# Kernel tuning notes

Measured on AMD Instinct MI355X. Metric: run time of the kernel, lower is better.

Reference implementation:

```python
import jax, jax.numpy as jnp
import numpy as np

TAU = 1.0
BASE = 7
NUM_TWISTS = 3
EPS = 1e-6

B, S, D, P, M = 4, 2048, 1024, 9, 256


def _rot(y, theta):
    # learned rotation in the (0,1) channel plane; theta broadcasts against y[..., 0]
    c, s = jnp.cos(theta), jnp.sin(theta)
    y0, y1 = y[..., 0], y[..., 1]
    r0 = (y0 * c - y1 * s)[..., None]
    r1 = (y0 * s + y1 * c)[..., None]
    return jnp.concatenate([r0, r1, y[..., 2:]], axis=-1)


def _mod_phase_norm(x, g, base=BASE):
    # RMS-normalize within channel groups defined by (channel index mod base)
    d = x.shape[-1]
    gid = jnp.arange(d) % base
    oh = jax.nn.one_hot(gid, base, dtype=x.dtype)           # [d, base]
    cnt = oh.sum(axis=0)                                    # [base]
    msq = (x * x) @ oh / cnt                                # [..., base]
    denom = jnp.sqrt(jnp.take(msq, gid, axis=-1) + EPS)     # [..., d]
    return x / denom * g


def setup_inputs() -> dict:
    key = jax.random.key(0)
    ks = jax.random.split(key, 16)
    w = lambda k, shape, scale: jax.random.normal(k, shape, dtype=jnp.float32) * scale
    u = jax.random.uniform(ks[1], (NUM_TWISTS + 1, B, S, P), dtype=jnp.float32,
                           minval=1e-6, maxval=1.0 - 1e-6)
    gumbel_noise = -jnp.log(-jnp.log(u))
    return {
        'x': w(ks[0], (B, S, D), 1.0),
        'gumbel_noise': gumbel_noise,
        'mixer_w': w(ks[2], (3, D), 0.5),
        'obs_W1': w(ks[3], (2 * D, M), (2 * D) ** -0.5),
        'obs_b1': jnp.zeros((M,), jnp.float32),
        'obs_th1': w(ks[4], (), 0.1),
        'obs_W2': w(ks[5], (M, P), M ** -0.5),
        'obs_b2': jnp.zeros((P,), jnp.float32),
        'obs_th2': w(ks[6], (), 0.1),
        'path_Wa': w(ks[7], (P, D, M), D ** -0.5),
        'path_ba': jnp.zeros((P, M), jnp.float32),
        'path_tha': w(ks[8], (P,), 0.1),
        'path_Wb': w(ks[9], (P, M, D), M ** -0.5),
        'path_bb': jnp.zeros((P, D), jnp.float32),
        'path_thb': w(ks[10], (P,), 0.1),
        'twist_W': w(ks[11], (D, D), D ** -0.5),
        'twist_b': jnp.zeros((D,), jnp.float32),
        'twist_th': w(ks[12], (), 0.1),
        'norm_g': jnp.ones((D,), jnp.float32),
    }


def reference(x, gumbel_noise, mixer_w, obs_W1, obs_b1, obs_th1, obs_W2, obs_b2,
              obs_th2, path_Wa, path_ba, path_tha, path_Wb, path_bb, path_thb,
              twist_W, twist_b, twist_th, norm_g):
    # neighbor mixer: per-channel 3-tap mix over sequence (zero-padded, non-causal)
    xp = jnp.pad(x, ((0, 0), (1, 1), (0, 0)))
    x_mixed = x * mixer_w[0] + xp[:, :-2] * mixer_w[1] + xp[:, 2:] * mixer_w[2]

    def observer_logits(collapsed):
        combined = jnp.concatenate([x_mixed, collapsed], axis=-1)      # [B,S,2D]
        h = jnp.tanh(_rot(combined @ obs_W1 + obs_b1, obs_th1))        # [B,S,M]
        return _rot(h @ obs_W2 + obs_b2, obs_th2)                      # [B,S,P]

    def path_outputs_fn(tin):
        h = _rot(jnp.einsum('bsd,pdm->bspm', tin, path_Wa) + path_ba, path_tha)
        return _rot(jnp.einsum('bspm,pmd->bspd', h, path_Wb) + path_bb, path_thb)

    collapsed = jnp.zeros_like(x_mixed)
    path_out = None
    for t in range(NUM_TWISTS):
        logits = observer_logits(collapsed)
        rw = jax.nn.softmax((logits + gumbel_noise[t]) / TAU, axis=-1)  # soft gumbel
        tin = x_mixed + _rot(collapsed @ twist_W + twist_b, twist_th)
        path_out = path_outputs_fn(tin)                                # [B,S,P,D]
        collapsed = _mod_phase_norm(jnp.einsum('bspd,bsp->bsd', path_out, rw), norm_g)

    # final hard (straight-through) gumbel routing, reusing last path_out
    final_logits = observer_logits(collapsed)
    soft = jax.nn.softmax((final_logits + gumbel_noise[NUM_TWISTS]) / TAU, axis=-1)
    hard = jax.nn.one_hot(jnp.argmax(soft, axis=-1), P, dtype=soft.dtype)
    rw_hard = hard + soft - jax.lax.stop_gradient(soft)
    final_collapsed = jnp.einsum('bspd,bsp->bsd', path_out, rw_hard)

    # dropout is identity in eval mode
    out = _mod_phase_norm(x + final_collapsed, norm_g)
    collapsed = _mod_phase_norm(collapsed, norm_g)
    return out, collapsed
```

## Files before the change

### kernel.cpp

```cpp
#include <hip/hip_runtime.h>
#include <hip/hip_bf16.h>

typedef unsigned short u16;
typedef short bf16x8 __attribute__((ext_vector_type(8)));
typedef float f32x4 __attribute__((ext_vector_type(4)));

constexpr int Dd = 1024, Pp = 9, Mm = 256, Nn = 8192, Kc = 2304;
constexpr float EPSf = 1e-6f;

__device__ __forceinline__ float bf2f(u16 u) {
    union { unsigned int u; float f; } v; v.u = ((unsigned int)u) << 16; return v.f;
}
__device__ __forceinline__ u16 f2bf(float f) {
    union { float f; unsigned int u; } v; v.f = f;
    unsigned int r = (v.u + 0x7FFFu + ((v.u >> 16) & 1u)) >> 16; return (u16)r;
}
__device__ __forceinline__ void split2(float v, u16& h, u16& l) {
    h = f2bf(v); l = f2bf(v - bf2f(h));
}
__device__ __forceinline__ void gld16(u16* lds, const u16* g) {
    __builtin_amdgcn_global_load_lds(
        (const __attribute__((address_space(1))) unsigned int*)g,
        (__attribute__((address_space(3))) unsigned int*)lds, 16, 0, 0);
}

__global__ void rotcopy_k(const float* __restrict__ src, float* __restrict__ dst,
                          int R, int C, const float* __restrict__ theta, int Pb)
{
    long total = (long)Pb * R * C;
    long idx = (long)blockIdx.x * 256 + threadIdx.x;
    if (idx >= total) return;
    int c = (int)(idx % C);
    long rp = idx / C;
    int r = (int)(rp % R);
    int pb = (int)(rp / R);
    float th = theta[pb];
    const float* s = src + ((long)pb * R + r) * C;
    float v;
    if (c == 0)      v = s[0] * cosf(th) - s[1] * sinf(th);
    else if (c == 1) v = s[0] * sinf(th) + s[1] * cosf(th);
    else             v = s[c];
    dst[idx] = v;
}

__global__ void splitW1_k(const float* __restrict__ W1, const float* __restrict__ th,
                          u16* __restrict__ h, u16* __restrict__ l)
{
    int idx = blockIdx.x * 256 + threadIdx.x;
    if (idx >= 256 * 2048) return;
    int k = idx & 2047, n = idx >> 11;
    float v;
    if (n == 0)      v = W1[(long)k * 256 + 0] * cosf(th[0]) - W1[(long)k * 256 + 1] * sinf(th[0]);
    else if (n == 1) v = W1[(long)k * 256 + 0] * sinf(th[0]) + W1[(long)k * 256 + 1] * cosf(th[0]);
    else             v = W1[(long)k * 256 + n];
    u16 hh, ll; split2(v, hh, ll); h[idx] = hh; l[idx] = ll;
}

__global__ void splitTW_k(const float* __restrict__ tW, const float* __restrict__ th,
                          u16* __restrict__ h, u16* __restrict__ l)
{
    int idx = blockIdx.x * 256 + threadIdx.x;
    if (idx >= 1024 * 1024) return;
    int k = idx & 1023, n = idx >> 10;
    float v;
    if (n == 0)      v = tW[(long)k * 1024 + 0] * cosf(th[0]) - tW[(long)k * 1024 + 1] * sinf(th[0]);
    else if (n == 1) v = tW[(long)k * 1024 + 0] * sinf(th[0]) + tW[(long)k * 1024 + 1] * cosf(th[0]);
    else             v = tW[(long)k * 1024 + n];
    u16 hh, ll; split2(v, hh, ll); h[idx] = hh; l[idx] = ll;
}

__global__ void splitWa_k(const float* __restrict__ Wa, const float* __restrict__ tha,
                          u16* __restrict__ h, u16* __restrict__ l)
{
    int idx = blockIdx.x * 256 + threadIdx.x;
    if (idx >= Kc * 1024) return;
    int k = idx & 1023, n = idx >> 10;
    int p = n >> 8, m = n & 255;
    const float* s = Wa + ((long)p * 1024 + k) * 256;
    float v;
    if (m == 0)      v = s[0] * cosf(tha[p]) - s[1] * sinf(tha[p]);
    else if (m == 1) v = s[0] * sinf(tha[p]) + s[1] * cosf(tha[p]);
    else             v = s[m];
    u16 hh, ll; split2(v, hh, ll); h[idx] = hh; l[idx] = ll;
}

__global__ void splitWb_k(const float* __restrict__ Wb, const float* __restrict__ thb,
                          u16* __restrict__ h, u16* __restrict__ l)
{
    int idx = blockIdx.x * 256 + threadIdx.x;
    if (idx >= 1024 * Kc) return;
    int n = idx / Kc;
    int k = idx - n * Kc;
    int p = k >> 8, m = k & 255;
    const float* s = Wb + ((long)p * 256 + m) * 1024;
    float v;
    if (n == 0)      v = s[0] * cosf(thb[p]) - s[1] * sinf(thb[p]);
    else if (n == 1) v = s[0] * sinf(thb[p]) + s[1] * cosf(thb[p]);
    else             v = s[n];
    u16 hh, ll; split2(v, hh, ll); h[idx] = hh; l[idx] = ll;
}

__global__ void mixer_k(const float* __restrict__ x, const float* __restrict__ mw,
                        u16* __restrict__ xmh, u16* __restrict__ xml)
{
    int idx = blockIdx.x * 256 + threadIdx.x;
    if (idx >= Nn * Dd / 4) return;
    int d4 = idx & (Dd / 4 - 1);
    int n = idx >> 8;
    int s = n & 2047;
    const float4* x4 = (const float4*)x;
    const float4* w4 = (const float4*)mw;
    float4 xc = x4[idx];
    float4 w0 = w4[d4], w1 = w4[(Dd / 4) + d4], w2 = w4[2 * (Dd / 4) + d4];
    float o[4];
    o[0] = xc.x * w0.x; o[1] = xc.y * w0.y; o[2] = xc.z * w0.z; o[3] = xc.w * w0.w;
    if (s > 0) {
        float4 xl = x4[idx - Dd / 4];
        o[0] += xl.x * w1.x; o[1] += xl.y * w1.y; o[2] += xl.z * w1.z; o[3] += xl.w * w1.w;
    }
    if (s < 2047) {
        float4 xr = x4[idx + Dd / 4];
        o[0] += xr.x * w2.x; o[1] += xr.y * w2.y; o[2] += xr.z * w2.z; o[3] += xr.w * w2.w;
    }
    ushort4 h4, l4;
    split2(o[0], h4.x, l4.x); split2(o[1], h4.y, l4.y);
    split2(o[2], h4.z, l4.z); split2(o[3], h4.w, l4.w);
    ((ushort4*)xmh)[idx] = h4; ((ushort4*)xml)[idx] = l4;
}

__global__ void tanh_k(const float* __restrict__ a, float* __restrict__ o, int total)
{
    int idx = blockIdx.x * 256 + threadIdx.x;
    if (idx < total) o[idx] = tanhf(a[idx]);
}

__global__ void addb_split_k(const u16* __restrict__ xmh, const u16* __restrict__ xml,
                             const float* __restrict__ tbr,
                             u16* __restrict__ th_, u16* __restrict__ tl_)
{
    int idx = blockIdx.x * 256 + threadIdx.x;
    if (idx >= Nn * Dd / 4) return;
    int d4 = idx & (Dd / 4 - 1);
    ushort4 xh = ((const ushort4*)xmh)[idx], xl = ((const ushort4*)xml)[idx];
    float4 b = ((const float4*)tbr)[d4];
    ushort4 h4, l4;
    split2(bf2f(xh.x) + bf2f(xl.x) + b.x, h4.x, l4.x);
    split2(bf2f(xh.y) + bf2f(xl.y) + b.y, h4.y, l4.y);
    split2(bf2f(xh.z) + bf2f(xl.z) + b.z, h4.z, l4.z);
    split2(bf2f(xh.w) + bf2f(xl.w) + b.w, h4.w, l4.w);
    ((ushort4*)th_)[idx] = h4; ((ushort4*)tl_)[idx] = l4;
}

template<int EPI>
__global__ __launch_bounds__(256, (EPI == 4) ? 2 : 3) void mgemm(
    const u16* __restrict__ Agh, const u16* __restrict__ Agl, int lda,
    const u16* __restrict__ Bgh, const u16* __restrict__ Bgl, int ldb,
    int K,
    float* __restrict__ Cf, u16* __restrict__ Coh, u16* __restrict__ Col, int ldc,
    const float* __restrict__ Cinit,
    const u16* __restrict__ CIh, const u16* __restrict__ CIl,
    const float* __restrict__ bias,
    const float* __restrict__ rwv,
    const float* __restrict__ rwv2,
    const float* __restrict__ bbrv)
{
    __shared__ u16 smem[16384];
    u16* As_h = smem;        u16* As_l = smem + 4096;
    u16* Bs_h = smem + 8192; u16* Bs_l = smem + 12288;
    const int tid = threadIdx.x, wave = tid >> 6, lane = tid & 63;
    const int nwg = gridDim.x * gridDim.y;
    const int flat = blockIdx.y * gridDim.x + blockIdx.x;
    const int q = nwg >> 3;
    const int l_ = (flat & 7) * q + (flat >> 3);
    const int r0 = (l_ / gridDim.x) * 128, c0 = (l_ % gridDim.x) * 128;
    const int srl = lane >> 2;
    const int ssl = ((lane & 3) ^ ((lane >> 3) & 3)) * 8;
    const int frl = lane & 15, kh = lane >> 4;
    const int sw  = (kh ^ ((frl >> 1) & 3)) * 8;
    const int arow0 = (wave >> 1) * 64, bcol0 = (wave & 1) * 64;
    const int w32 = wave * 32;

    f32x4 acc[4][4] = {};

    auto kstep = [&](f32x4 (&ac)[4][4], int k0) {
        {
            const long ga0 = (long)(r0 + w32 + srl) * lda + k0 + ssl;
            gld16(&As_h[w32 * 32],        Agh + ga0);
            gld16(&As_h[(w32 + 16) * 32], Agh + ga0 + 16L * lda);
            gld16(&As_l[w32 * 32],        Agl + ga0);
            gld16(&As_l[(w32 + 16) * 32], Agl + ga0 + 16L * lda);
            const long gb0 = (long)(c0 + w32 + srl) * ldb + k0 + ssl;
            gld16(&Bs_h[w32 * 32],        Bgh + gb0);
            gld16(&Bs_h[(w32 + 16) * 32], Bgh + gb0 + 16L * ldb);
            gld16(&Bs_l[w32 * 32],        Bgl + gb0);
            gld16(&Bs_l[(w32 + 16) * 32], Bgl + gb0 + 16L * ldb);
        }
        __syncthreads();
        bf16x8 ah[4], al[4];
#pragma unroll
        for (int f = 0; f < 4; ++f) {
            int ao = (arow0 + f * 16 + frl) * 32 + sw;
            ah[f] = *(const bf16x8*)&As_h[ao];
            al[f] = *(const bf16x8*)&As_l[ao];
        }
#pragma unroll
        for (int j = 0; j < 4; ++j) {
            int bo = (bcol0 + j * 16 + frl) * 32 + sw;
            bf16x8 bh = *(const bf16x8*)&Bs_h[bo];
            bf16x8 bl = *(const bf16x8*)&Bs_l[bo];
#pragma unroll
            for (int i = 0; i < 4; ++i) {
                ac[i][j] = __builtin_amdgcn_mfma_f32_16x16x32_bf16(ah[i], bh, ac[i][j], 0, 0, 0);
                ac[i][j] = __builtin_amdgcn_mfma_f32_16x16x32_bf16(ah[i], bl, ac[i][j], 0, 0, 0);
                ac[i][j] = __builtin_amdgcn_mfma_f32_16x16x32_bf16(al[i], bh, ac[i][j], 0, 0, 0);
            }
        }
        __syncthreads();
    };

    if constexpr (EPI == 4) {
#pragma unroll 1
        for (int p = 0; p < 9; ++p) {
            f32x4 acc2[4][4] = {};
#pragma unroll 1
            for (int ks = 0; ks < 8; ++ks) kstep(acc2, p * 256 + ks * 32);
#pragma unroll
            for (int i = 0; i < 4; ++i)
#pragma unroll
                for (int reg = 0; reg < 4; ++reg) {
                    float w = rwv[(long)(r0 + arow0 + i * 16 + kh * 4 + reg) * 9 + p];
#pragma unroll
                    for (int j = 0; j < 4; ++j) acc[i][j][reg] += w * acc2[i][j][reg];
                }
        }
    } else {
#pragma unroll 1
        for (int k0 = 0; k0 < K; k0 += 32) kstep(acc, k0);
    }

#pragma unroll
    for (int i = 0; i < 4; ++i)
#pragma unroll
        for (int reg = 0; reg < 4; ++reg) {
            const int r = r0 + arow0 + i * 16 + kh * 4 + reg;
#pragma unroll
            for (int j = 0; j < 4; ++j) {
                const int c = c0 + bcol0 + j * 16 + frl;
                float v = acc[i][j][reg];
                if constexpr (EPI == 0) {
                    Cf[(long)r * ldc + c] = v + bias[c];
                } else if constexpr (EPI == 1) {
                    Cf[(long)r * ldc + c] = tanhf(v + Cinit[(long)r * ldc + c]);
                } else if constexpr (EPI == 2) {
                    long o = (long)r * ldc + c;
                    v += bf2f(CIh[o]) + bf2f(CIl[o]) + bias[c];
                    u16 h, l; split2(v, h, l); Coh[o] = h; Col[o] = l;
                } else if constexpr (EPI == 3) {
                    long o = (long)r * ldc + c;
                    v = (v + bias[c]) * rwv[(long)r * 9 + (c >> 8)];
                    u16 h, l; split2(v, h, l); Coh[o] = h; Col[o] = l;
                } else if constexpr (EPI == 4) {
#pragma unroll
                    for (int p = 0; p < 9; ++p) v += rwv2[(long)r * 9 + p] * bbrv[p * 1024 + c];
                    Cf[(long)r * ldc + c] = v;
                } else {
#pragma unroll
                    for (int p = 0; p < 9; ++p) v += rwv[(long)r * 9 + p] * bbrv[p * 1024 + c];
                    Cf[(long)r * ldc + c] = v;
                }
            }
        }
}

__global__ void logits_k(const float* __restrict__ h, const float* __restrict__ W2r,
                         const float* __restrict__ b2r, const float* __restrict__ gum,
                         float* __restrict__ rwA, float* __restrict__ rwH,
                         const float* __restrict__ rwS, int hard)
{
    __shared__ float hs[Mm];
    __shared__ float lg[16];
    int n = blockIdx.x;
    for (int i = threadIdx.x; i < Mm; i += 64) hs[i] = h[(long)n * Mm + i];
    __syncthreads();
    if (threadIdx.x < Pp) {
        int p = threadIdx.x;
        float acc = b2r[p];
        for (int m = 0; m < Mm; ++m) acc += hs[m] * W2r[m * Pp + p];
        lg[p] = acc + gum[(long)n * Pp + p];
    }
    __syncthreads();
    if (threadIdx.x == 0) {
        float mx = lg[0]; int am = 0;
#pragma unroll
        for (int p = 1; p < Pp; ++p) if (lg[p] > mx) { mx = lg[p]; am = p; }
        if (hard) {
#pragma unroll
            for (int p = 0; p < Pp; ++p) {
                rwA[(long)n * Pp + p] = (p == am) ? 1.f / rwS[(long)n * Pp + p] : 0.f;
                rwH[(long)n * Pp + p] = (p == am) ? 1.f : 0.f;
            }
        } else {
            float e[Pp]; float ssum = 0.f;
#pragma unroll
            for (int p = 0; p < Pp; ++p) { e[p] = expf(lg[p] - mx); ssum += e[p]; }
#pragma unroll
            for (int p = 0; p < Pp; ++p) rwA[(long)n * Pp + p] = e[p] / ssum;
        }
    }
}

template<int INSPLIT, int OUTSPLIT>
__global__ void norm_k(const float* __restrict__ in,
                       const u16* __restrict__ inh, const u16* __restrict__ inl,
                       const float* __restrict__ add, const float* __restrict__ g,
                       float* __restrict__ outf, u16* __restrict__ oh, u16* __restrict__ ol)
{
    __shared__ float sb[256][8];
    __shared__ float dn[8];
    int n = blockIdx.x;
    int t = threadIdx.x;
    float v[4];
#pragma unroll
    for (int j = 0; j < 7; ++j) sb[t][j] = 0.f;
#pragma unroll
    for (int i = 0; i < 4; ++i) {
        int d = t + i * 256;
        long o = (long)n * Dd + d;
        float xv = INSPLIT ? (bf2f(inh[o]) + bf2f(inl[o])) : in[o];
        if (add) xv += add[o];
        v[i] = xv;
        sb[t][d % 7] += xv * xv;
    }
    __syncthreads();
    for (int st = 128; st >= 1; st >>= 1) {
        if (t < st) {
#pragma unroll
            for (int j = 0; j < 7; ++j) sb[t][j] += sb[t + st][j];
        }
        __syncthreads();
    }
    if (t < 7) {
        const float cnt = (t < 2) ? 147.f : 146.f;
        dn[t] = 1.f / sqrtf(sb[0][t] / cnt + EPSf);
    }
    __syncthreads();
#pragma unroll
    for (int i = 0; i < 4; ++i) {
        int d = t + i * 256;
        long o = (long)n * Dd + d;
        float ov = v[i] * dn[d % 7] * g[d];
        if (OUTSPLIT) { u16 h, l; split2(ov, h, l); oh[o] = h; ol[o] = l; }
        else outf[o] = ov;
    }
}

static inline int cdiv(long a, long b) { return (int)((a + b - 1) / b); }

extern "C" void kernel_launch(void* const* d_in, const int* in_sizes, int n_in,
                              void* d_out, int out_size, void* d_ws, size_t ws_size,
                              hipStream_t stream)
{
    const float* x    = (const float*)d_in[0];
    const float* gum  = (const float*)d_in[1];
    const float* mw   = (const float*)d_in[2];
    const float* W1   = (const float*)d_in[3];
    const float* b1   = (const float*)d_in[4];
    const float* th1  = (const float*)d_in[5];
    const float* W2   = (const float*)d_in[6];
    const float* b2   = (const float*)d_in[7];
    const float* th2  = (const float*)d_in[8];
    const float* Wa   = (const float*)d_in[9];
    const float* ba   = (const float*)d_in[10];
    const float* tha  = (const float*)d_in[11];
    const float* Wb   = (const float*)d_in[12];
    const float* bbv  = (const float*)d_in[13];
    const float* thb  = (const float*)d_in[14];
    const float* tW   = (const float*)d_in[15];
    const float* tb   = (const float*)d_in[16];
    const float* tth  = (const float*)d_in[17];
    const float* gnorm = (const float*)d_in[18];

    char* cur = (char*)d_ws;
    auto alloc = [&](size_t bytes) -> void* {
        void* r = (void*)cur; cur += (bytes + 255) & ~(size_t)255; return r;
    };
    void* region = alloc((size_t)Nn * Dd * 4);
    float* craw = (float*)region;
    float* hbuf = (float*)region;
    u16*   tinh = (u16*)region;
    u16*   tinl = tinh + (size_t)Nn * Dd;
    float* zx   = (float*)alloc((size_t)Nn * Mm * 4);
    float* rwS  = (float*)alloc((size_t)Nn * Pp * 4);
    float* rwD  = (float*)alloc((size_t)Nn * Pp * 4);
    float* rwH  = (float*)alloc((size_t)Nn * Pp * 4);
    u16* xmh  = (u16*)alloc((size_t)Nn * Dd * 2);
    u16* xml  = (u16*)alloc((size_t)Nn * Dd * 2);
    u16* colh = (u16*)alloc((size_t)Nn * Dd * 2);
    u16* coll = (u16*)alloc((size_t)Nn * Dd * 2);
    u16* hph  = (u16*)alloc((size_t)Nn * Kc * 2);
    u16* hpl  = (u16*)alloc((size_t)Nn * Kc * 2);
    u16* W1th = (u16*)alloc(256 * 2048 * 2);
    u16* W1tl = (u16*)alloc(256 * 2048 * 2);
    u16* tWth = (u16*)alloc(1024 * 1024 * 2);
    u16* tWtl = (u16*)alloc(1024 * 1024 * 2);
    u16* Wath = (u16*)alloc((size_t)Kc * 1024 * 2);
    u16* Watl = (u16*)alloc((size_t)Kc * 1024 * 2);
    u16* Wbth = (u16*)alloc((size_t)1024 * Kc * 2);
    u16* Wbtl = (u16*)alloc((size_t)1024 * Kc * 2);
    float* W2r = (float*)alloc(256 * 9 * 4);
    float* b1r = (float*)alloc(256 * 4);
    float* b2r = (float*)alloc(16 * 4);
    float* bac = (float*)alloc(Kc * 4);
    float* bbr = (float*)alloc(Pp * 1024 * 4);
    float* tbr = (float*)alloc(1024 * 4);
    if ((size_t)(cur - (char*)d_ws) > ws_size) return;

    float* out0 = (float*)d_out;
    float* out1 = out0 + (long)Nn * Dd;

    splitW1_k<<<2048, 256, 0, stream>>>(W1, th1, W1th, W1tl);
    splitTW_k<<<4096, 256, 0, stream>>>(tW, tth, tWth, tWtl);
    splitWa_k<<<cdiv((long)Kc * 1024, 256), 256, 0, stream>>>(Wa, tha, Wath, Watl);
    splitWb_k<<<cdiv((long)1024 * Kc, 256), 256, 0, stream>>>(Wb, thb, Wbth, Wbtl);
    rotcopy_k<<<cdiv(256L * 9, 256), 256, 0, stream>>>(W2, W2r, 256, 9, th2, 1);
    rotcopy_k<<<1, 256, 0, stream>>>(b1, b1r, 1, 256, th1, 1);
    rotcopy_k<<<1, 256, 0, stream>>>(b2, b2r, 1, 9, th2, 1);
    rotcopy_k<<<cdiv((long)Pp * Mm, 256), 256, 0, stream>>>(ba, bac, 1, 256, tha, 9);
    rotcopy_k<<<cdiv((long)Pp * 1024, 256), 256, 0, stream>>>(bbv, bbr, 1, 1024, thb, 9);
    rotcopy_k<<<cdiv(1024L, 256), 256, 0, stream>>>(tb, tbr, 1, 1024, tth, 1);

    mixer_k<<<Nn * Dd / 4 / 256, 256, 0, stream>>>(x, mw, xmh, xml);

    mgemm<0><<<dim3(2, 64), 256, 0, stream>>>(
        xmh, xml, 1024, W1th, W1tl, 2048, 1024,
        zx, nullptr, nullptr, 256, nullptr, nullptr, nullptr, b1r, nullptr, nullptr, nullptr);

    for (int t = 0; t < 3; ++t) {
        if (t == 0) {
            tanh_k<<<cdiv((long)Nn * Mm, 256), 256, 0, stream>>>(zx, hbuf, Nn * Mm);
        } else {
            mgemm<1><<<dim3(2, 64), 256, 0, stream>>>(
                colh, coll, 1024, W1th + 1024, W1tl + 1024, 2048, 1024,
                hbuf, nullptr, nullptr, 256, zx, nullptr, nullptr, nullptr, nullptr, nullptr, nullptr);
        }
        logits_k<<<Nn, 64, 0, stream>>>(hbuf, W2r, b2r, gum + (long)t * Nn * Pp,
                                        rwS, nullptr, nullptr, 0);
        if (t == 0) {
            addb_split_k<<<Nn * Dd / 4 / 256, 256, 0, stream>>>(xmh, xml, tbr, tinh, tinl);
        } else {
            mgemm<2><<<dim3(8, 64), 256, 0, stream>>>(
                colh, coll, 1024, tWth, tWtl, 1024, 1024,
                nullptr, tinh, tinl, 1024, nullptr, xmh, xml, tbr, nullptr, nullptr, nullptr);
        }
        mgemm<3><<<dim3(18, 64), 256, 0, stream>>>(
            tinh, tinl, 1024, Wath, Watl, 1024, 1024,
            nullptr, hph, hpl, Kc, nullptr, nullptr, nullptr, bac, rwS, nullptr, nullptr);
        mgemm<5><<<dim3(8, 64), 256, 0, stream>>>(
            hph, hpl, Kc, Wbth, Wbtl, Kc, Kc,
            craw, nullptr, nullptr, 1024, nullptr, nullptr, nullptr, nullptr, rwS, nullptr, bbr);
        norm_k<0, 1><<<Nn, 256, 0, stream>>>(craw, nullptr, nullptr, nullptr, gnorm,
                                             nullptr, colh, coll);
    }

    mgemm<1><<<dim3(2, 64), 256, 0, stream>>>(
        colh, coll, 1024, W1th + 1024, W1tl + 1024, 2048, 1024,
        hbuf, nullptr, nullptr, 256, zx, nullptr, nullptr, nullptr, nullptr, nullptr, nullptr);
    logits_k<<<Nn, 64, 0, stream>>>(hbuf, W2r, b2r, gum + 3L * Nn * Pp,
                                    rwD, rwH, rwS, 1);
    mgemm<4><<<dim3(8, 64), 256, 0, stream>>>(
        hph, hpl, Kc, Wbth, Wbtl, Kc, Kc,
        craw, nullptr, nullptr, 1024, nullptr, nullptr, nullptr, nullptr, rwD, rwH, bbr);
    norm_k<0, 0><<<Nn, 256, 0, stream>>>(craw, nullptr, nullptr, x, gnorm, out0, nullptr, nullptr);
    norm_k<1, 0><<<Nn, 256, 0, stream>>>(nullptr, colh, coll, nullptr, gnorm, out1, nullptr, nullptr);
}
```

Before: 1.448 ms.

## Double-buffer LDS tiles in split-bf16 GEMM to overlap loads with MFMA

Restructures the GEMM main loop to use two LDS buffers. The next K-tile's global-to-LDS loads are issued before the current tile is computed, and explicit vmcnt waits plus barriers order the two. The aim is to hide global load latency behind the triple-MFMA compute. The per-path weighted flush for EPI 4 moves into the unified loop. LDS use doubles to 64KB per block and launch bounds drop to 2 blocks per CU for all variants, which may reduce occupancy.

```diff
diff --git a/kernel.cpp b/kernel.cpp
--- a/kernel.cpp
+++ b/kernel.cpp
@@ -152,7 +152,7 @@
 }
 
 template<int EPI>
-__global__ __launch_bounds__(256, (EPI == 4) ? 2 : 3) void mgemm(
+__global__ __launch_bounds__(256, 2) void mgemm(
     const u16* __restrict__ Agh, const u16* __restrict__ Agl, int lda,
     const u16* __restrict__ Bgh, const u16* __restrict__ Bgl, int ldb,
     int K,
@@ -164,9 +164,7 @@
     const float* __restrict__ rwv2,
     const float* __restrict__ bbrv)
 {
-    __shared__ u16 smem[16384];
-    u16* As_h = smem;        u16* As_l = smem + 4096;
-    u16* Bs_h = smem + 8192; u16* Bs_l = smem + 12288;
+    __shared__ u16 smem[2][16384];
     const int tid = threadIdx.x, wave = tid >> 6, lane = tid & 63;
     const int nwg = gridDim.x * gridDim.y;
     const int flat = blockIdx.y * gridDim.x + blockIdx.x;
@@ -181,21 +179,33 @@
     const int w32 = wave * 32;
 
     f32x4 acc[4][4] = {};
-
-    auto kstep = [&](f32x4 (&ac)[4][4], int k0) {
-        {
-            const long ga0 = (long)(r0 + w32 + srl) * lda + k0 + ssl;
-            gld16(&As_h[w32 * 32],        Agh + ga0);
-            gld16(&As_h[(w32 + 16) * 32], Agh + ga0 + 16L * lda);
-            gld16(&As_l[w32 * 32],        Agl + ga0);
-            gld16(&As_l[(w32 + 16) * 32], Agl + ga0 + 16L * lda);
-            const long gb0 = (long)(c0 + w32 + srl) * ldb + k0 + ssl;
-            gld16(&Bs_h[w32 * 32],        Bgh + gb0);
-            gld16(&Bs_h[(w32 + 16) * 32], Bgh + gb0 + 16L * ldb);
-            gld16(&Bs_l[w32 * 32],        Bgl + gb0);
-            gld16(&Bs_l[(w32 + 16) * 32], Bgl + gb0 + 16L * ldb);
-        }
-        __syncthreads();
+    f32x4 acc2[4][4];
+    if constexpr (EPI == 4) {
+#pragma unroll
+        for (int i = 0; i < 4; ++i)
+#pragma unroll
+            for (int j = 0; j < 4; ++j) acc2[i][j] = f32x4{0.f, 0.f, 0.f, 0.f};
+    }
+
+    auto STAGE = [&](int buf, int k0) {
+        u16* base = &smem[buf][0];
+        u16* As_h = base;        u16* As_l = base + 4096;
+        u16* Bs_h = base + 8192; u16* Bs_l = base + 12288;
+        const long ga0 = (long)(r0 + w32 + srl) * lda + k0 + ssl;
+        gld16(&As_h[w32 * 32],        Agh + ga0);
+        gld16(&As_h[(w32 + 16) * 32], Agh + ga0 + 16L * lda);
+        gld16(&As_l[w32 * 32],        Agl + ga0);
+        gld16(&As_l[(w32 + 16) * 32], Agl + ga0 + 16L * lda);
+        const long gb0 = (long)(c0 + w32 + srl) * ldb + k0 + ssl;
+        gld16(&Bs_h[w32 * 32],        Bgh + gb0);
+        gld16(&Bs_h[(w32 + 16) * 32], Bgh + gb0 + 16L * ldb);
+        gld16(&Bs_l[w32 * 32],        Bgl + gb0);
+        gld16(&Bs_l[(w32 + 16) * 32], Bgl + gb0 + 16L * ldb);
+    };
+    auto COMPUTE = [&](int buf, f32x4 (&ac)[4][4]) {
+        u16* base = &smem[buf][0];
+        u16* As_h = base;        u16* As_l = base + 4096;
+        u16* Bs_h = base + 8192; u16* Bs_l = base + 12288;
         bf16x8 ah[4], al[4];
 #pragma unroll
         for (int f = 0; f < 4; ++f) {
@@ -215,27 +225,50 @@
                 ac[i][j] = __builtin_amdgcn_mfma_f32_16x16x32_bf16(al[i], bh, ac[i][j], 0, 0, 0);
             }
         }
-        __syncthreads();
     };
-
-    if constexpr (EPI == 4) {
+    auto FLUSH = [&](int p) {
+#pragma unroll
+        for (int i = 0; i < 4; ++i)
+#pragma unroll
+            for (int reg = 0; reg < 4; ++reg) {
+                float w = rwv[(long)(r0 + arow0 + i * 16 + kh * 4 + reg) * 9 + p];
+#pragma unroll
+                for (int j = 0; j < 4; ++j) {
+                    acc[i][j][reg] += w * acc2[i][j][reg];
+                    acc2[i][j][reg] = 0.f;
+                }
+            }
+    };
+
+    const int NT = K / 32;
+    STAGE(0, 0);
 #pragma unroll 1
-        for (int p = 0; p < 9; ++p) {
-            f32x4 acc2[4][4] = {};
-#pragma unroll 1
-            for (int ks = 0; ks < 8; ++ks) kstep(acc2, p * 256 + ks * 32);
-#pragma unroll
-            for (int i = 0; i < 4; ++i)
-#pragma unroll
-                for (int reg = 0; reg < 4; ++reg) {
-                    float w = rwv[(long)(r0 + arow0 + i * 16 + kh * 4 + reg) * 9 + p];
-#pragma unroll
-                    for (int j = 0; j < 4; ++j) acc[i][j][reg] += w * acc2[i][j][reg];
-                }
-        }
-    } else {
-#pragma unroll 1
-        for (int k0 = 0; k0 < K; k0 += 32) kstep(acc, k0);
+    for (int t = 0; t < NT; t += 2) {
+        STAGE(1, (t + 1) * 32);
+        asm volatile("s_waitcnt vmcnt(8)" ::: "memory");
+        __builtin_amdgcn_sched_barrier(0);
+        __builtin_amdgcn_s_barrier();
+        __builtin_amdgcn_sched_barrier(0);
+        if constexpr (EPI == 4) COMPUTE(0, acc2); else COMPUTE(0, acc);
+        __builtin_amdgcn_sched_barrier(0);
+        __builtin_amdgcn_s_barrier();
+        __builtin_amdgcn_sched_barrier(0);
+        if (t + 2 < NT) {
+            STAGE(0, (t + 2) * 32);
+            asm volatile("s_waitcnt vmcnt(8)" ::: "memory");
+        } else {
+            asm volatile("s_waitcnt vmcnt(0)" ::: "memory");
+        }
+        __builtin_amdgcn_sched_barrier(0);
+        __builtin_amdgcn_s_barrier();
+        __builtin_amdgcn_sched_barrier(0);
+        if constexpr (EPI == 4) COMPUTE(1, acc2); else COMPUTE(1, acc);
+        __builtin_amdgcn_sched_barrier(0);
+        __builtin_amdgcn_s_barrier();
+        __builtin_amdgcn_sched_barrier(0);
+        if constexpr (EPI == 4) {
+            if (((t + 1) & 7) == 7) FLUSH((t + 1) >> 3);
+        }
     }
 
 #pragma unroll
```

New measurement: 1.434 ms. Within noise of the previous version (-1.0%).
